# Kernel optimization log

Measured on AMD Instinct MI355X. Metric: run time of the kernel, lower is better.

## Reference

```python
import jax, jax.numpy as jnp
import numpy as np

H = 256                      # neural_renderer default image_size
VIEW_ANGLE = 30.0            # neural_renderer default viewing_angle (deg)
SIGMA = 1e-4                 # soft-rasterizer sharpness for the silhouette
DIST_THRESH = 6.0
NUM_V, NUM_F = 512, 1024


def setup_inputs() -> dict:
    key = jax.random.key(0)
    k1, k2, k3 = jax.random.split(key, 3)
    v = jax.random.uniform(k1, (NUM_V, 3), jnp.float32)
    # normalization from Model.__init__
    v = v - v.min(0)[None, :]
    v = v / jnp.abs(v).max()
    v = v * 2.0
    v = v - v.max(0)[None, :] / 2.0
    vertices = v[None]                                    # [1, V, 3]
    faces = jax.random.randint(k2, (1, NUM_F, 3), 0, NUM_V, jnp.int32)
    image_ref = (jax.random.uniform(k3, (H, H)) > 0.5).astype(jnp.float32)
    camera_position = jnp.array([6.0, 10.0, -14.0], jnp.float32)
    return {"vertices": vertices, "faces": faces,
            "image_ref": image_ref, "camera_position": camera_position}


def _render_silhouette(vertices, faces, eye):
    # --- look_at transform (at=origin, up=+y), as in neural_renderer ---
    def _norm(a):
        return a / (jnp.linalg.norm(a) + 1e-8)
    z_axis = _norm(-eye)
    up = jnp.array([0.0, 1.0, 0.0], eye.dtype)
    x_axis = _norm(jnp.cross(up, z_axis))
    y_axis = _norm(jnp.cross(z_axis, x_axis))
    R = jnp.stack([x_axis, y_axis, z_axis])               # [3, 3]
    v = (vertices - eye) @ R.T                            # [V, 3] camera space
    # --- perspective projection, viewing_angle = 30 deg ---
    t = np.float32(np.tan(np.deg2rad(VIEW_ANGLE)))
    z = v[:, 2]
    xy = v[:, :2] / (z[:, None] * t + 1e-8)               # NDC in [-1, 1]
    tri = xy[faces]                                       # [F, 3, 2]
    tri_z = z[faces]                                      # [F, 3]
    valid = jnp.all(tri_z > 1e-3, axis=1)                 # cull faces behind cam
    # --- pixel grid (row 0 = top, like the rendered image) ---
    c = (jnp.arange(H, dtype=jnp.float32) + 0.5) / H * 2.0 - 1.0
    qx, qy = jnp.meshgrid(c, -c)                          # [H, H]
    q = jnp.stack([qx.ravel(), qy.ravel()], -1)           # [H*W, 2]

    def edge_dist(a, b):
        # signed distance of every pixel to edge a->b, [H*W, F]
        e = b - a                                         # [F, 2]
        inv_len = 1.0 / (jnp.sqrt(jnp.sum(e * e, -1)) + 1e-8)
        cross = (e[None, :, 0] * (q[:, None, 1] - a[None, :, 1])
                 - e[None, :, 1] * (q[:, None, 0] - a[None, :, 0]))
        return cross * inv_len[None, :]

    d0 = edge_dist(tri[:, 0], tri[:, 1])
    d1 = edge_dist(tri[:, 1], tri[:, 2])
    d2 = edge_dist(tri[:, 2], tri[:, 0])
    dmin = jnp.minimum(jnp.minimum(d0, d1), d2)
    dmax = jnp.maximum(jnp.maximum(d0, d1), d2)
    # positive inside the triangle regardless of winding
    dist = jnp.maximum(dmin, -dmax)                       # [H*W, F]
    prob = jax.nn.sigmoid(dist * jnp.abs(dist) / SIGMA)
    prob = jnp.where(valid[None, :], prob, 0.0)
    prob = jnp.clip(prob, 0.0, 1.0 - 1e-6)
    # silhouette alpha = 1 - prod_f (1 - prob_f), computed in log space
    alpha = 1.0 - jnp.exp(jnp.sum(jnp.log1p(-prob), axis=1))
    return alpha.reshape(H, H)[None]                      # [1, H, W]


def reference(vertices, faces, image_ref, camera_position):
    image = _render_silhouette(vertices[0], faces[0], camera_position)
    distance = jnp.linalg.norm(camera_position)
    distance_penalty = jax.nn.relu(DIST_THRESH - distance)
    loss = jnp.sum((image_ref[None] - image) ** 2) * (1.0 + distance_penalty)
    return loss
```

## Files before the change

### kernel.cpp

```cpp
#include <hip/hip_runtime.h>
#include <math.h>

#define NUM_V 512
#define NUM_F 1024
#define IMG_H 256
#define NPIX (IMG_H*IMG_H)
#define NCHUNK 16
#define FPC (NUM_F/NCHUNK)
#define TAN_T 0.57735026919f
#define LOG_EPS  -13.8155106f
#define DCULL_S  -3.72f

__global__ __launch_bounds__(256, 8) void render_kernel(
    const float* __restrict__ verts,
    const int*   __restrict__ faces,
    const float* __restrict__ cam,
    float* __restrict__ slices,
    int*   __restrict__ cnt,
    float* __restrict__ out)
{
    __shared__ float sx[NUM_V], sy[NUM_V], sz[NUM_V];
    __shared__ float4 sfA[FPC+4], sfB[FPC+4];
    __shared__ float  sfC[FPC+4];
    __shared__ int scnt;
    const int tid   = threadIdx.x;
    const int chunk = blockIdx.x & (NCHUNK-1);
    const int tile  = blockIdx.x / NCHUNK;

    if (blockIdx.x == 0 && tid == 0) out[0] = 0.0f;
    if (tid == 0) scnt = 0;

    const float ex = cam[0], ey = cam[1], ez = cam[2];
    float inv = 1.0f / (sqrtf(ex*ex + ey*ey + ez*ez) + 1e-8f);
    const float zx = -ex*inv, zy = -ey*inv, zz = -ez*inv;
    float xxr = zz, xyr = 0.0f, xzr = -zx;
    inv = 1.0f / (sqrtf(xxr*xxr + xyr*xyr + xzr*xzr) + 1e-8f);
    const float xx = xxr*inv, xy = xyr*inv, xz = xzr*inv;
    float yxr = zy*xz - zz*xy;
    float yyr = zz*xx - zx*xz;
    float yzr = zx*xy - zy*xx;
    inv = 1.0f / (sqrtf(yxr*yxr + yyr*yyr + yzr*yzr) + 1e-8f);
    const float yx = yxr*inv, yy = yyr*inv, yz = yzr*inv;

    for (int v = tid; v < NUM_V; v += 256) {
        float px = verts[3*v+0] - ex;
        float py = verts[3*v+1] - ey;
        float pz = verts[3*v+2] - ez;
        float vx = xx*px + xy*py + xz*pz;
        float vy = yx*px + yy*py + yz*pz;
        float vz = zx*px + zy*py + zz*pz;
        float denom = 1.0f / (vz*TAN_T + 1e-8f);
        sx[v] = vx*denom;
        sy[v] = vy*denom;
        sz[v] = vz;
    }
    __syncthreads();

    const int j0 = (tile & 15) * 16;
    const int i0 = (tile >> 4) * 16;
    const float xL = (j0 + 0.5f )*(2.0f/IMG_H) - 1.0f;
    const float xR = (j0 + 15.5f)*(2.0f/IMG_H) - 1.0f;
    const float yT = 1.0f - (i0 + 0.5f )*(2.0f/IMG_H);
    const float yB = 1.0f - (i0 + 15.5f)*(2.0f/IMG_H);

    if (tid < FPC) {
        const int f = chunk*FPC + tid;
        int i0f = faces[3*f+0], i1f = faces[3*f+1], i2f = faces[3*f+2];
        float ax = sx[i0f], ay = sy[i0f], z0 = sz[i0f];
        float bx = sx[i1f], by = sy[i1f], z1 = sz[i1f];
        float cx = sx[i2f], cy = sy[i2f], z2 = sz[i2f];
        bool keep = (z0 > 0.001f && z1 > 0.001f && z2 > 0.001f);

        float A[3], B[3], C[3];
        const float px_[3] = {ax, bx, cx}, py_[3] = {ay, by, cy};
        const float qx_[3] = {bx, cx, ax}, qy_[3] = {by, cy, ay};
        #pragma unroll
        for (int k = 0; k < 3; ++k) {
            float eex = qx_[k] - px_[k];
            float eey = qy_[k] - py_[k];
            float il = 100.0f / (sqrtf(eex*eex + eey*eey) + 1e-8f);
            A[k] = eex*il;
            B[k] = eey*il;
            C[k] = (eex*py_[k] - eey*px_[k])*il;
        }

        if (keep) {
            float minmx = 3.0e38f, maxmn = -3.0e38f;
            #pragma unroll
            for (int k = 0; k < 3; ++k) {
                float dTL = A[k]*yT - B[k]*xL - C[k];
                float dTR = A[k]*yT - B[k]*xR - C[k];
                float dBL = A[k]*yB - B[k]*xL - C[k];
                float dBR = A[k]*yB - B[k]*xR - C[k];
                float mx = fmaxf(fmaxf(dTL, dTR), fmaxf(dBL, dBR));
                float mn = fminf(fminf(dTL, dTR), fminf(dBL, dBR));
                minmx = fminf(minmx, mx);
                maxmn = fmaxf(maxmn, mn);
            }
            keep = !((minmx <= DCULL_S) && (maxmn >= -DCULL_S));
        }
        if (keep) {
            int s = atomicAdd(&scnt, 1);
            sfA[s] = make_float4(A[0], B[0], C[0], A[1]);
            sfB[s] = make_float4(B[1], C[1], A[2], B[2]);
            sfC[s] = C[2];
        }
    }
    __syncthreads();

    const int n = scnt;
    if (tid == 0) cnt[tile*NCHUNK + chunk] = n;
    if (n == 0) return;

    const int npad = (4 - (n & 3)) & 3;
    if (tid < npad) {
        const int s = n + tid;
        sfA[s] = make_float4(0.0f, 0.0f, 1e30f, 0.0f);
        sfB[s] = make_float4(0.0f, -1e30f, 0.0f, 0.0f);
        sfC[s] = 0.0f;
    }
    __syncthreads();
    const int ng = (n + 3) & ~3;

    const int w = tid >> 6, l = tid & 63;
    const int lj = (w & 1)*8 + (l & 7);
    const int li = (w >> 1)*8 + (l >> 3);
    const int j = j0 + lj, i = i0 + li;
    const float qx = (j + 0.5f)*(2.0f/IMG_H) - 1.0f;
    const float qy = 1.0f - (i + 0.5f)*(2.0f/IMG_H);

    float acc = 0.0f;
    for (int g = 0; g < ng; g += 4) {
        float dist4[4];
        #pragma unroll
        for (int u = 0; u < 4; ++u) {
            float4 w0 = sfA[g+u];
            float4 w1 = sfB[g+u];
            float  c2 = sfC[g+u];
            float d0 = fmaf(w0.x, qy, -fmaf(w0.y, qx, w0.z));
            float d1 = fmaf(w0.w, qy, -fmaf(w1.x, qx, w1.y));
            float d2 = fmaf(w1.z, qy, -fmaf(w1.w, qx, c2));
            float dmin = fminf(fminf(d0, d1), d2);
            float dmax = fmaxf(fmaxf(d0, d1), d2);
            dist4[u] = fmaxf(dmin, -dmax);
        }
        float gm = fmaxf(fmaxf(dist4[0], dist4[1]), fmaxf(dist4[2], dist4[3]));
        if (__any(gm > DCULL_S)) {
            #pragma unroll
            for (int u = 0; u < 4; ++u) {
                float dist = dist4[u];
                float s  = dist * fabsf(dist);
                float e2 = __builtin_exp2f(-fabsf(s) * 1.44269504f);
                float lg = __builtin_log2f(1.0f + e2);
                float sp = fmaf(lg, 0.69314718f, fmaxf(s, 0.0f));
                acc += fmaxf(-sp, LOG_EPS);
            }
        }
    }
    slices[(tile*NCHUNK + chunk)*256 + li*16 + lj] = acc;
}

__global__ __launch_bounds__(256) void finalize_kernel(
    const float* __restrict__ image_ref,
    const float* __restrict__ slices,
    const int*   __restrict__ cnt,
    const float* __restrict__ cam,
    float* __restrict__ out)
{
    __shared__ float wsum[4];
    const int tid  = threadIdx.x;
    const int tile = blockIdx.x;
    const int j0 = (tile & 15) * 16;
    const int i0 = (tile >> 4) * 16;
    const int li = tid >> 4, lj = tid & 15;
    const int p  = (i0 + li)*IMG_H + (j0 + lj);

    float lsum = 0.0f;
    #pragma unroll
    for (int c = 0; c < NCHUNK; ++c) {
        if (cnt[tile*NCHUNK + c] > 0)
            lsum += slices[(tile*NCHUNK + c)*256 + tid];
    }
    float alpha = 1.0f - __expf(lsum);
    float diff  = image_ref[p] - alpha;
    float sq = diff * diff;

    #pragma unroll
    for (int off = 32; off > 0; off >>= 1) sq += __shfl_down(sq, off, 64);
    if ((tid & 63) == 0) wsum[tid >> 6] = sq;
    __syncthreads();
    if (tid == 0) {
        float ex = cam[0], ey = cam[1], ez = cam[2];
        float dist = sqrtf(ex*ex + ey*ey + ez*ez);
        float pen = fmaxf(6.0f - dist, 0.0f);
        float bs = (wsum[0] + wsum[1]) + (wsum[2] + wsum[3]);
        atomicAdd(out, bs * (1.0f + pen));
    }
}

extern "C" void kernel_launch(void* const* d_in, const int* in_sizes, int n_in,
                              void* d_out, int out_size, void* d_ws, size_t ws_size,
                              hipStream_t stream)
{
    const float* verts     = (const float*)d_in[0];
    const int*   faces     = (const int*)  d_in[1];
    const float* image_ref = (const float*)d_in[2];
    const float* cam       = (const float*)d_in[3];

    float* slices = (float*)d_ws;
    int*   cnt    = (int*)((char*)d_ws + 256*NCHUNK*256*sizeof(float));
    float* out    = (float*)d_out;

    render_kernel  <<<256*NCHUNK, 256, 0, stream>>>(verts, faces, cam,
                                                    slices, cnt, out);
    finalize_kernel<<<256,        256, 0, stream>>>(image_ref, slices, cnt,
                                                    cam, out);
}
```

Before: 79.51 us.

## Process four tiles per render block to amortize vertex projection setup

```diff
diff --git a/kernel.cpp b/kernel.cpp
--- a/kernel.cpp
+++ b/kernel.cpp
@@ -4,12 +4,15 @@
 #define NUM_V 512
 #define NUM_F 1024
 #define IMG_H 256
-#define NPIX (IMG_H*IMG_H)
 #define NCHUNK 16
 #define FPC (NUM_F/NCHUNK)
+#define NTILE 256
+#define TPB 4
+#define NGRP (NTILE/TPB)
 #define TAN_T 0.57735026919f
 #define LOG_EPS  -13.8155106f
 #define DCULL_S  -3.72f
+
 
 __global__ __launch_bounds__(256, 8) void render_kernel(
     const float* __restrict__ verts,
@@ -23,12 +26,12 @@
     __shared__ float4 sfA[FPC+4], sfB[FPC+4];
     __shared__ float  sfC[FPC+4];
     __shared__ int scnt;
+
     const int tid   = threadIdx.x;
     const int chunk = blockIdx.x & (NCHUNK-1);
-    const int tile  = blockIdx.x / NCHUNK;
+    const int grp   = blockIdx.x >> 4;
 
     if (blockIdx.x == 0 && tid == 0) out[0] = 0.0f;
-    if (tid == 0) scnt = 0;
 
     const float ex = cam[0], ey = cam[1], ez = cam[2];
     float inv = 1.0f / (sqrtf(ex*ex + ey*ey + ez*ez) + 1e-8f);
@@ -56,22 +59,15 @@
     }
     __syncthreads();
 
-    const int j0 = (tile & 15) * 16;
-    const int i0 = (tile >> 4) * 16;
-    const float xL = (j0 + 0.5f )*(2.0f/IMG_H) - 1.0f;
-    const float xR = (j0 + 15.5f)*(2.0f/IMG_H) - 1.0f;
-    const float yT = 1.0f - (i0 + 0.5f )*(2.0f/IMG_H);
-    const float yB = 1.0f - (i0 + 15.5f)*(2.0f/IMG_H);
-
+    float A[3], B[3], C[3];
+    bool valid = false;
     if (tid < FPC) {
         const int f = chunk*FPC + tid;
         int i0f = faces[3*f+0], i1f = faces[3*f+1], i2f = faces[3*f+2];
         float ax = sx[i0f], ay = sy[i0f], z0 = sz[i0f];
         float bx = sx[i1f], by = sy[i1f], z1 = sz[i1f];
         float cx = sx[i2f], cy = sy[i2f], z2 = sz[i2f];
-        bool keep = (z0 > 0.001f && z1 > 0.001f && z2 > 0.001f);
-
-        float A[3], B[3], C[3];
+        valid = (z0 > 0.001f && z1 > 0.001f && z2 > 0.001f);
         const float px_[3] = {ax, bx, cx}, py_[3] = {ay, by, cy};
         const float qx_[3] = {bx, cx, ax}, qy_[3] = {by, cy, ay};
         #pragma unroll
@@ -83,81 +79,95 @@
             B[k] = eey*il;
             C[k] = (eex*py_[k] - eey*px_[k])*il;
         }
-
-        if (keep) {
+    }
+
+    const int w = tid >> 6, l = tid & 63;
+    const int lj = (w & 1)*8 + (l & 7);
+    const int li = (w >> 1)*8 + (l >> 3);
+
+    for (int k = 0; k < TPB; ++k) {
+        const int tile = grp + NGRP*k;
+        const int j0 = (tile & 15) * 16;
+        const int i0 = (tile >> 4) * 16;
+
+        __syncthreads();
+        if (tid == 0) scnt = 0;
+        __syncthreads();
+
+        if (tid < FPC && valid) {
+            const float xL = (j0 + 0.5f )*(2.0f/IMG_H) - 1.0f;
+            const float xR = (j0 + 15.5f)*(2.0f/IMG_H) - 1.0f;
+            const float yT = 1.0f - (i0 + 0.5f )*(2.0f/IMG_H);
+            const float yB = 1.0f - (i0 + 15.5f)*(2.0f/IMG_H);
             float minmx = 3.0e38f, maxmn = -3.0e38f;
             #pragma unroll
-            for (int k = 0; k < 3; ++k) {
-                float dTL = A[k]*yT - B[k]*xL - C[k];
-                float dTR = A[k]*yT - B[k]*xR - C[k];
-                float dBL = A[k]*yB - B[k]*xL - C[k];
-                float dBR = A[k]*yB - B[k]*xR - C[k];
+            for (int e = 0; e < 3; ++e) {
+                float dTL = A[e]*yT - B[e]*xL - C[e];
+                float dTR = A[e]*yT - B[e]*xR - C[e];
+                float dBL = A[e]*yB - B[e]*xL - C[e];
+                float dBR = A[e]*yB - B[e]*xR - C[e];
                 float mx = fmaxf(fmaxf(dTL, dTR), fmaxf(dBL, dBR));
                 float mn = fminf(fminf(dTL, dTR), fminf(dBL, dBR));
                 minmx = fminf(minmx, mx);
                 maxmn = fmaxf(maxmn, mn);
             }
-            keep = !((minmx <= DCULL_S) && (maxmn >= -DCULL_S));
-        }
-        if (keep) {
-            int s = atomicAdd(&scnt, 1);
-            sfA[s] = make_float4(A[0], B[0], C[0], A[1]);
-            sfB[s] = make_float4(B[1], C[1], A[2], B[2]);
-            sfC[s] = C[2];
-        }
-    }
-    __syncthreads();
-
-    const int n = scnt;
-    if (tid == 0) cnt[tile*NCHUNK + chunk] = n;
-    if (n == 0) return;
-
-    const int npad = (4 - (n & 3)) & 3;
-    if (tid < npad) {
-        const int s = n + tid;
-        sfA[s] = make_float4(0.0f, 0.0f, 1e30f, 0.0f);
-        sfB[s] = make_float4(0.0f, -1e30f, 0.0f, 0.0f);
-        sfC[s] = 0.0f;
-    }
-    __syncthreads();
-    const int ng = (n + 3) & ~3;
-
-    const int w = tid >> 6, l = tid & 63;
-    const int lj = (w & 1)*8 + (l & 7);
-    const int li = (w >> 1)*8 + (l >> 3);
-    const int j = j0 + lj, i = i0 + li;
-    const float qx = (j + 0.5f)*(2.0f/IMG_H) - 1.0f;
-    const float qy = 1.0f - (i + 0.5f)*(2.0f/IMG_H);
-
-    float acc = 0.0f;
-    for (int g = 0; g < ng; g += 4) {
-        float dist4[4];
-        #pragma unroll
-        for (int u = 0; u < 4; ++u) {
-            float4 w0 = sfA[g+u];
-            float4 w1 = sfB[g+u];
-            float  c2 = sfC[g+u];
-            float d0 = fmaf(w0.x, qy, -fmaf(w0.y, qx, w0.z));
-            float d1 = fmaf(w0.w, qy, -fmaf(w1.x, qx, w1.y));
-            float d2 = fmaf(w1.z, qy, -fmaf(w1.w, qx, c2));
-            float dmin = fminf(fminf(d0, d1), d2);
-            float dmax = fmaxf(fmaxf(d0, d1), d2);
-            dist4[u] = fmaxf(dmin, -dmax);
-        }
-        float gm = fmaxf(fmaxf(dist4[0], dist4[1]), fmaxf(dist4[2], dist4[3]));
-        if (__any(gm > DCULL_S)) {
+            bool keep = !((minmx <= DCULL_S) && (maxmn >= -DCULL_S));
+            if (keep) {
+                int s = atomicAdd(&scnt, 1);
+                sfA[s] = make_float4(A[0], B[0], C[0], A[1]);
+                sfB[s] = make_float4(B[1], C[1], A[2], B[2]);
+                sfC[s] = C[2];
+            }
+        }
+        __syncthreads();
+
+        const int n = scnt;
+        if (tid == 0) cnt[tile*NCHUNK + chunk] = n;
+        if (n == 0) continue;
+
+        const int npad = (4 - (n & 3)) & 3;
+        if (tid < npad) {
+            const int s = n + tid;
+            sfA[s] = make_float4(0.0f, 0.0f, 1e30f, 0.0f);
+            sfB[s] = make_float4(0.0f, -1e30f, 0.0f, 0.0f);
+            sfC[s] = 0.0f;
+        }
+        __syncthreads();
+        const int ng = (n + 3) & ~3;
+
+        const float qx = (j0 + lj + 0.5f)*(2.0f/IMG_H) - 1.0f;
+        const float qy = 1.0f - (i0 + li + 0.5f)*(2.0f/IMG_H);
+
+        float acc = 0.0f;
+        for (int g = 0; g < ng; g += 4) {
+            float dist4[4];
             #pragma unroll
             for (int u = 0; u < 4; ++u) {
-                float dist = dist4[u];
-                float s  = dist * fabsf(dist);
-                float e2 = __builtin_exp2f(-fabsf(s) * 1.44269504f);
-                float lg = __builtin_log2f(1.0f + e2);
-                float sp = fmaf(lg, 0.69314718f, fmaxf(s, 0.0f));
-                acc += fmaxf(-sp, LOG_EPS);
-            }
-        }
-    }
-    slices[(tile*NCHUNK + chunk)*256 + li*16 + lj] = acc;
+                float4 w0 = sfA[g+u];
+                float4 w1 = sfB[g+u];
+                float  c2 = sfC[g+u];
+                float d0 = fmaf(w0.x, qy, -fmaf(w0.y, qx, w0.z));
+                float d1 = fmaf(w0.w, qy, -fmaf(w1.x, qx, w1.y));
+                float d2 = fmaf(w1.z, qy, -fmaf(w1.w, qx, c2));
+                float dmin = fminf(fminf(d0, d1), d2);
+                float dmax = fmaxf(fmaxf(d0, d1), d2);
+                dist4[u] = fmaxf(dmin, -dmax);
+            }
+            float gm = fmaxf(fmaxf(dist4[0], dist4[1]), fmaxf(dist4[2], dist4[3]));
+            if (__any(gm > DCULL_S)) {
+                #pragma unroll
+                for (int u = 0; u < 4; ++u) {
+                    float dist = dist4[u];
+                    float s  = dist * fabsf(dist);
+                    float e2 = __builtin_exp2f(-fabsf(s) * 1.44269504f);
+                    float lg = __builtin_log2f(1.0f + e2);
+                    float sp = fmaf(lg, 0.69314718f, fmaxf(s, 0.0f));
+                    acc += fmaxf(-sp, LOG_EPS);
+                }
+            }
+        }
+        slices[(tile*NCHUNK + chunk)*256 + li*16 + lj] = acc;
+    }
 }
 
 __global__ __launch_bounds__(256) void finalize_kernel(
@@ -208,11 +218,11 @@
     const float* cam       = (const float*)d_in[3];
 
     float* slices = (float*)d_ws;
-    int*   cnt    = (int*)((char*)d_ws + 256*NCHUNK*256*sizeof(float));
+    int*   cnt    = (int*)((char*)d_ws + NTILE*NCHUNK*256*4);
     float* out    = (float*)d_out;
 
-    render_kernel  <<<256*NCHUNK, 256, 0, stream>>>(verts, faces, cam,
-                                                    slices, cnt, out);
-    finalize_kernel<<<256,        256, 0, stream>>>(image_ref, slices, cnt,
-                                                    cam, out);
+    render_kernel  <<<NGRP*NCHUNK, 256, 0, stream>>>(verts, faces, cam,
+                                                     slices, cnt, out);
+    finalize_kernel<<<NTILE,       256, 0, stream>>>(image_ref, slices, cnt,
+                                                     cam, out);
 }
```

Result: slower. 83.50 us (+5.0%).
